# Performance work log

Hardware: AMD Instinct MI355X
Metric: run time of the kernel (lower is better)

## Reference

```python
import jax, jax.numpy as jnp
import numpy as np

B = 65536
N_DIM = 16
K = 64
HIDDEN = 256
IDX_COPIED = np.arange(0, N_DIM, 2)      # mask == 0
IDX_TRANS = np.arange(1, N_DIM, 2)       # mask == 1
T = len(IDX_TRANS)                        # n_dim_transformed = 8
OUT = T * (2 * K + 1)                     # 1032


def setup_inputs() -> dict:
    key = jax.random.key(0)
    ks = jax.random.split(key, 7)
    def lin_init(k, fan_in, shape):
        s = 1.0 / np.sqrt(fan_in)
        return jax.random.uniform(k, shape, minval=-s, maxval=s, dtype=jnp.float32)
    x = jax.random.uniform(ks[0], (B, N_DIM), dtype=jnp.float32)  # inputs in [0,1)
    W1 = lin_init(ks[1], T, (T, HIDDEN)); b1 = lin_init(ks[2], T, (HIDDEN,))
    W2 = lin_init(ks[3], HIDDEN, (HIDDEN, HIDDEN)); b2 = lin_init(ks[4], HIDDEN, (HIDDEN,))
    W3 = lin_init(ks[5], HIDDEN, (HIDDEN, OUT)); b3 = lin_init(ks[6], HIDDEN, (OUT,))
    return {"x": x, "W1": W1, "b1": b1, "W2": W2, "b2": b2, "W3": W3, "b3": b3}


def reference(x, W1, b1, W2, b2, W3, b3):
    xc = x[:, IDX_COPIED]                 # [B, T] copied dims
    xt = x[:, IDX_TRANS]                  # [B, T] transformed dims
    # FCNN as built by torch: Linear, Linear, ReLU, Linear (no ReLU after 1st)
    h = xc @ W1 + b1
    h = jax.nn.relu(h @ W2 + b2)
    params = h @ W3 + b3                  # [B, T*(2K+1)]

    Vun = params[:, : T * (K + 1)].reshape(B, T, K + 1)
    Wun = params[:, T * (K + 1):].reshape(B, T, K)
    Wb = jax.nn.softmax(Wun, axis=-1)     # bin widths [B,T,K]

    expV = jnp.exp(Vun)                   # [B,T,K+1]
    denom = jnp.sum(0.5 * (expV[..., :-1] + expV[..., 1:]) * Wb, axis=-1, keepdims=True)
    V = expV / denom                      # normalized vertex heights [B,T,K+1]

    Wcum = jnp.cumsum(Wb, axis=-1)        # [B,T,K]
    b = jnp.argmax((Wcum > xt[..., None]).astype(jnp.int32), axis=-1, keepdims=True)  # bin index [B,T,1]
    Wcum_pad = jnp.pad(Wcum, ((0, 0), (0, 0), (1, 0)))

    g = lambda a, idx: jnp.take_along_axis(a, idx, axis=-1)
    Wb_b = g(Wb, b)
    alpha = (xt[..., None] - g(Wcum_pad, b)) / Wb_b   # relative position in bin

    Cint = 0.5 * (V[..., :-1] + V[..., 1:]) * Wb      # per-bin CDF mass [B,T,K]
    Cint_cum = jnp.pad(jnp.cumsum(Cint, axis=-1), ((0, 0), (0, 0), (1, 0)))

    Vb = g(V, b); Vb1 = g(V, b + 1)
    C = (0.5 * alpha**2 * (Vb1 - Vb) * Wb_b + alpha * Vb * Wb_b + g(Cint_cum, b))[..., 0]  # [B,T]

    z = jnp.zeros_like(x).at[:, IDX_COPIED].set(xc).at[:, IDX_TRANS].set(C)
    z = jnp.where(z > 1.0, 1.0, z)

    q = Vb + alpha * (Vb1 - Vb)           # linear interp of density
    log_J = jnp.sum(jnp.log(q)[..., 0], axis=-1)      # [B]
    return z, log_J
```

## Files before the change

kernel.cpp:

```cpp
#include <hip/hip_runtime.h>

typedef short s16x8 __attribute__((ext_vector_type(8)));
typedef float fx4 __attribute__((ext_vector_type(4)));

#define NROWS 65536
#define LOG2E 1.4426950408889634f
#define LN2   0.6931471805599453f

#define MFMA(a, b, c) __builtin_amdgcn_mfma_f32_16x16x32_bf16((a), (b), (c), 0, 0, 0)

__device__ __forceinline__ unsigned short f2bf(float f) {
  union { float f; unsigned u; } v; v.f = f;
  unsigned r = v.u + 0x7fffu + ((v.u >> 16) & 1u);
  return (unsigned short)(r >> 16);
}

__device__ __forceinline__ float fexp2(float x) {
  float r; asm("v_exp_f32 %0, %1" : "=v"(r) : "v"(x)); return r;
}
__device__ __forceinline__ float flog2(float x) {
  float r; asm("v_log_f32 %0, %1" : "=v"(r) : "v"(x)); return r;
}
__device__ __forceinline__ float frcp(float x) {
  float r; asm("v_rcp_f32 %0, %1" : "=v"(r) : "v"(x)); return r;
}

__global__ void pack_weights(const float* __restrict__ W1, const float* __restrict__ b1,
                             const float* __restrict__ W2, const float* __restrict__ b2,
                             const float* __restrict__ W3,
                             unsigned short* __restrict__ W12P, float* __restrict__ b12,
                             unsigned short* __restrict__ W3Q, unsigned short* __restrict__ W3X) {
  int blk = blockIdx.x, tid = threadIdx.x;
  if (blk < 1024) {
    int i3 = blk * 256 + tid;
    int e = i3 & 7, lane = (i3 >> 3) & 63, nti = (i3 >> 9) & 7, ks = (i3 >> 12) & 7, t = i3 >> 15;
    int m = lane & 15, kc = lane >> 4;
    int k = ks * 32 + kc * 8 + e;
    int g = m >> 2, rg = m & 3;
    int c = (nti < 4) ? (t * 65 + 16 * g + nti * 4 + rg)
                      : (520 + t * 64 + 16 * g + (nti - 4) * 4 + rg);
    W3Q[i3] = f2bf(W3[k * 1032 + c] * LOG2E);
  } else if (blk < 1040) {
    int ix = (blk - 1024) * 256 + tid;
    int e = ix & 7, n = (ix >> 3) & 15, kc = (ix >> 7) & 3, ks = ix >> 9;
    int k = ks * 32 + kc * 8 + e;
    float v = (n < 8) ? (W3[k * 1032 + n * 65 + 64] * LOG2E) : 0.0f;
    W3X[ix] = f2bf(v);
  } else if (blk < 1048) {
    int k = blk - 1040, c = tid;
    float s = 0.0f;
    for (int m = 0; m < 256; m++) s += W1[k * 256 + m] * W2[m * 256 + c];
    W12P[c * 8 + k] = f2bf(s);
  } else {
    int c = tid;
    float s = b2[c];
    for (int m = 0; m < 256; m++) s += b1[m] * W2[m * 256 + c];
    b12[c] = s;
  }
}

__global__ __launch_bounds__(256, 2) void fused_pwquad(
    const float* __restrict__ x, const float* __restrict__ b3,
    const unsigned short* __restrict__ W12P, const float* __restrict__ b12,
    const unsigned short* __restrict__ W3Q, const unsigned short* __restrict__ W3X,
    float* __restrict__ out)
{
  __shared__ char smem_all[75776];
  const int tid  = threadIdx.x;
  const int w    = tid >> 6;
  const int lane = tid & 63;
  const int kc   = lane >> 4;
  const int l15  = lane & 15;
  const int r0   = blockIdx.x * 128 + w * 32;

  char*  smem  = smem_all + w * 18944;
  char*  H     = smem;
  float* b3V   = (float*)smem;
  float* b3W   = (float*)(smem + 2176);
  char*  XC    = smem + 16384;
  float* xt_s  = (float*)(smem + 16896);
  float* v64_s = (float*)(smem + 17920);

  {
    const float4* xin = (const float4*)(x + (size_t)r0 * 16);
    #pragma unroll
    for (int i = 0; i < 2; i++) {
      int f = i * 64 + lane;
      float4 v = xin[f];
      int row = f >> 2, q = f & 3;
      out[(size_t)(r0 + row) * 16 + 4 * q + 0] = fminf(v.x, 1.0f);
      out[(size_t)(r0 + row) * 16 + 4 * q + 2] = fminf(v.z, 1.0f);
      unsigned pk = (unsigned)f2bf(v.x) | ((unsigned)f2bf(v.z) << 16);
      *(unsigned*)(XC + row * 16 + q * 4) = pk;
      float2 t2; t2.x = v.y; t2.y = v.w;
      *(float2*)(xt_s + row * 8 + 2 * q) = t2;
    }
  }

  {
    s16x8 ah[2] = {};
    if (kc == 0) {
      #pragma unroll
      for (int mi = 0; mi < 2; mi++) ah[mi] = *(const s16x8*)(XC + (mi * 16 + l15) * 16);
    }
    #pragma unroll
    for (int c = 0; c < 4; c++) {
      s16x8 bh[4];
      #pragma unroll
      for (int nt = 0; nt < 4; nt++)
        bh[nt] = *(const s16x8*)(W12P + (size_t)(c * 64 + nt * 16 + l15) * 8);
      fx4 acc[2][4];
      #pragma unroll
      for (int mi = 0; mi < 2; mi++)
        #pragma unroll
        for (int nt = 0; nt < 4; nt++) acc[mi][nt] = (fx4){0.f, 0.f, 0.f, 0.f};
      #pragma unroll
      for (int mi = 0; mi < 2; mi++)
        #pragma unroll
        for (int nt = 0; nt < 4; nt++) acc[mi][nt] = MFMA(ah[mi], bh[nt], acc[mi][nt]);
      #pragma unroll
      for (int nt = 0; nt < 4; nt++) {
        int col = c * 64 + nt * 16 + l15;
        float bias = b12[col];
        #pragma unroll
        for (int mi = 0; mi < 2; mi++) {
          #pragma unroll
          for (int rg = 0; rg < 4; rg++) {
            int row = mi * 16 + kc * 4 + rg;
            float v = fmaxf(acc[mi][nt][rg] + bias, 0.0f);
            int byte = (row << 9) + (col << 1);
            byte ^= ((row & 7) << 4);
            *(unsigned short*)(H + byte) = f2bf(v);
          }
        }
      }
    }
  }

  s16x8 a3[2][8];
  #pragma unroll
  for (int mi = 0; mi < 2; mi++) {
    #pragma unroll
    for (int ks = 0; ks < 8; ks++) {
      int row = mi * 16 + l15;
      int byte = (row << 9) + ks * 64 + (kc << 4);
      byte ^= ((row & 7) << 4);
      a3[mi][ks] = *(const s16x8*)(H + byte);
    }
  }
  {
    fx4 ax0 = (fx4){0.f, 0.f, 0.f, 0.f}, ax1 = ax0;
    #pragma unroll
    for (int ks = 0; ks < 8; ks++) {
      s16x8 bx = *(const s16x8*)(W3X + ((size_t)(ks * 4 + kc) * 16 + l15) * 8);
      ax0 = MFMA(a3[0][ks], bx, ax0);
      ax1 = MFMA(a3[1][ks], bx, ax1);
    }
    if (l15 < 8) {
      float bias = b3[l15 * 65 + 64] * LOG2E;
      #pragma unroll
      for (int rg = 0; rg < 4; rg++) {
        v64_s[(kc * 4 + rg) * 8 + l15]      = ax0[rg] + bias;
        v64_s[(16 + kc * 4 + rg) * 8 + l15] = ax1[rg] + bias;
      }
    }
  }

  #pragma unroll
  for (int t = 0; t < 8; t++) {
    b3V[t * 68 + lane] = b3[t * 65 + lane] * LOG2E;
    b3W[t * 64 + lane] = b3[520 + t * 64 + lane] * LOG2E;
  }

  const char* wp = (const char*)W3Q + (size_t)lane * 16;

  s16x8 F0[8], F1[8];
  #pragma unroll
  for (int nti = 0; nti < 8; nti++) F0[nti] = *(const s16x8*)(wp + nti * 1024);

  float ljacc[2] = {0.0f, 0.0f};
  const fx4 Z = (fx4){0.f, 0.f, 0.f, 0.f};

  #pragma unroll 1
  for (int t = 0; t < 8; t++) {
    const char* wk = wp + (size_t)t * 65536;

    fx4 accT[8][2];

    {
      #pragma unroll
      for (int nti = 0; nti < 8; nti++) F1[nti] = *(const s16x8*)(wk + 8192 + nti * 1024);
      __builtin_amdgcn_s_setprio(1);
      #pragma unroll
      for (int nti = 0; nti < 8; nti++) {
        accT[nti][0] = MFMA(F0[nti], a3[0][0], Z);
        accT[nti][1] = MFMA(F0[nti], a3[1][0], Z);
      }
      __builtin_amdgcn_s_setprio(0);
      #pragma unroll
      for (int nti = 0; nti < 8; nti++) F0[nti] = *(const s16x8*)(wk + 16384 + nti * 1024);
      __builtin_amdgcn_s_setprio(1);
      #pragma unroll
      for (int nti = 0; nti < 8; nti++) {
        accT[nti][0] = MFMA(F1[nti], a3[0][1], accT[nti][0]);
        accT[nti][1] = MFMA(F1[nti], a3[1][1], accT[nti][1]);
      }
      __builtin_amdgcn_s_setprio(0);
    }
    #pragma unroll
    for (int kp = 1; kp < 4; kp++) {
      const char* e0 = wk + kp * 16384;
      #pragma unroll
      for (int nti = 0; nti < 8; nti++) F1[nti] = *(const s16x8*)(e0 + 8192 + nti * 1024);
      __builtin_amdgcn_s_setprio(1);
      #pragma unroll
      for (int nti = 0; nti < 8; nti++) {
        accT[nti][0] = MFMA(F0[nti], a3[0][2 * kp], accT[nti][0]);
        accT[nti][1] = MFMA(F0[nti], a3[1][2 * kp], accT[nti][1]);
      }
      __builtin_amdgcn_s_setprio(0);
      if (kp < 3 || t < 7) {
        #pragma unroll
        for (int nti = 0; nti < 8; nti++) F0[nti] = *(const s16x8*)(e0 + 16384 + nti * 1024);
      }
      __builtin_amdgcn_s_setprio(1);
      #pragma unroll
      for (int nti = 0; nti < 8; nti++) {
        accT[nti][0] = MFMA(F1[nti], a3[0][2 * kp + 1], accT[nti][0]);
        accT[nti][1] = MFMA(F1[nti], a3[1][2 * kp + 1], accT[nti][1]);
      }
      __builtin_amdgcn_s_setprio(0);
    }

    fx4 vb[4], wb[4];
    {
      const float* bV = b3V + t * 68 + 16 * kc;
      const float* bW = b3W + t * 64 + 16 * kc;
      #pragma unroll
      for (int i = 0; i < 4; i++) { vb[i] = *(const fx4*)(bV + 4 * i); wb[i] = *(const fx4*)(bW + 4 * i); }
    }
    float xtv_p[2], vlast_p[2];
    xtv_p[0]   = xt_s[l15 * 8 + t];        xtv_p[1]   = xt_s[(16 + l15) * 8 + t];
    vlast_p[0] = v64_s[l15 * 8 + t];       vlast_p[1] = v64_s[(16 + l15) * 8 + t];

    #pragma unroll
    for (int mi = 0; mi < 2; mi++) {
      int row = mi * 16 + l15;
      float xtv   = xtv_p[mi];
      float vlast = vlast_p[mi];

      float wj[16];
      #pragma unroll
      for (int i = 0; i < 4; i++)
        #pragma unroll
        for (int j = 0; j < 4; j++)
          wj[4 * i + j] = fexp2(accT[4 + i][mi][j] + wb[i][j]);

      float esum = 0.0f;
      #pragma unroll
      for (int j = 0; j < 16; j++) esum += wj[j];

      float g0 = __shfl(esum, l15, 64);
      float g1 = __shfl(esum, l15 + 16, 64);
      float g2 = __shfl(esum, l15 + 32, 64);
      float g3 = __shfl(esum, l15 + 48, 64);
      float S = (g0 + g1) + (g2 + g3);
      float ebase = 0.0f;
      if (kc > 0) ebase += g0;
      if (kc > 1) ebase += g1;
      if (kc > 2) ebase += g2;
      float xs = xtv * S;

      float v0my = accT[0][mi][0] + vb[0][0];
      float vnext = __shfl(v0my, l15 + (((kc + 1) & 3) << 4), 64);
      if (kc == 3) vnext = vlast;

      float run = ebase;
      float evc = fexp2(v0my);
      float dl = 0.0f, cpart = 0.0f;
      float wpadc = 0.0f, wbbc = 1.0f, evb = evc, evb1 = evc;
      float ev15 = evc, ev16 = evc;
      int jcap = 16;
      #pragma unroll
      for (int j = 0; j < 16; j++) {
        float vr = (j < 15) ? (accT[(j + 1) >> 2][mi][(j + 1) & 3] + vb[(j + 1) >> 2][(j + 1) & 3])
                            : vnext;
        float evn = fexp2(vr);
        float wbj = wj[j];
        float nw = run + wbj;
        bool hit = (run <= xs) && (nw > xs);
        if (hit) { wpadc = run; wbbc = wbj; evb = evc; evb1 = evn; cpart = dl; jcap = j; }
        dl += (evc + evn) * wbj;
        if (j == 15) { ev15 = evc; ev16 = evn; }
        run = nw; evc = evn;
      }
      int bloc = (jcap < 16) ? (kc * 16 + jcap) : 64;
      int bmin = min(bloc, __shfl_xor(bloc, 16, 64));
      bmin = min(bmin, __shfl_xor(bmin, 32, 64));

      float d0 = __shfl(dl, l15, 64);
      float d1 = __shfl(dl, l15 + 16, 64);
      float d2 = __shfl(dl, l15 + 32, 64);
      float d3 = __shfl(dl, l15 + 48, 64);
      float dltot = (d0 + d1) + (d2 + d3);
      float cbase2 = 0.0f;
      if (kc > 0) cbase2 += d0;
      if (kc > 1) cbase2 += d1;
      if (kc > 2) cbase2 += d2;

      if (bmin == 64) {
        wbbc = wj[15];
        wpadc = run - wbbc;
        evb = ev15; evb1 = ev16;
        cpart = dl - (ev15 + ev16) * wj[15];
        bmin = 63;
      }

      if (kc == (bmin >> 4)) {
        float alpha = (xs - wpadc) * frcp(wbbc);
        float Cnum = (alpha * (evb + 0.5f * alpha * (evb1 - evb))) * wbbc
                   + 0.5f * (cbase2 + cpart);
        out[(size_t)(r0 + row) * 16 + 2 * t + 1] = fminf(2.0f * Cnum * frcp(dltot), 1.0f);
        float qn = evb + alpha * (evb1 - evb);
        ljacc[mi] += flog2(qn) - (flog2(dltot) - 1.0f - flog2(S));
      }
    }
  }

  #pragma unroll
  for (int mi = 0; mi < 2; mi++) {
    float v = ljacc[mi];
    v += __shfl_xor(v, 16, 64);
    v += __shfl_xor(v, 32, 64);
    if (kc == 0) out[(size_t)NROWS * 16 + r0 + mi * 16 + l15] = v * LN2;
  }
}

extern "C" void kernel_launch(void* const* d_in, const int* in_sizes, int n_in,
                              void* d_out, int out_size, void* d_ws, size_t ws_size,
                              hipStream_t stream) {
  const float* x  = (const float*)d_in[0];
  const float* W1 = (const float*)d_in[1];
  const float* b1 = (const float*)d_in[2];
  const float* W2 = (const float*)d_in[3];
  const float* b2 = (const float*)d_in[4];
  const float* W3 = (const float*)d_in[5];
  const float* b3 = (const float*)d_in[6];

  unsigned short* W12P = (unsigned short*)d_ws;
  float*          b12  = (float*)((char*)d_ws + 4096);
  unsigned short* W3Q  = (unsigned short*)((char*)d_ws + 5120);
  unsigned short* W3X  = (unsigned short*)((char*)d_ws + 529408);

  pack_weights<<<dim3(1049), dim3(256), 0, stream>>>(W1, b1, W2, b2, W3, W12P, b12, W3Q, W3X);
  fused_pwquad<<<dim3(NROWS / 128), dim3(256), 0, stream>>>(
      x, b3, W12P, b12, W3Q, W3X, (float*)d_out);
}
```

Baseline: 56.95 us.

## Stage W3 weight fragments through double-buffered LDS shared across the block's waves

Before, each of the four waves streamed its own copy of the packed W3 bf16 fragments from global memory into registers for the final-layer MFMA loop. Now the block loads each 8 KB k-slice once, cooperatively at 32 bytes per thread, into one of two LDS buffers. Each slice is prefetched two steps ahead into registers, and the waves read their MFMA fragments from LDS. This removes the 4x redundant global/L2 weight traffic per block. In exchange it adds a block-wide barrier after every k-step (64 per block) and extra LDS traffic, and it reuses LDS space left by the finished hidden-activation stage as the two buffers.

```diff
diff --git a/kernel.cpp b/kernel.cpp
--- a/kernel.cpp
+++ b/kernel.cpp
@@ -23,6 +23,10 @@
 }
 __device__ __forceinline__ float frcp(float x) {
   float r; asm("v_rcp_f32 %0, %1" : "=v"(r) : "v"(x)); return r;
+}
+
+__device__ __forceinline__ void bar_lds() {
+  asm volatile("s_waitcnt lgkmcnt(0)\n\ts_barrier" ::: "memory");
 }
 
 __global__ void pack_weights(const float* __restrict__ W1, const float* __restrict__ b1,
@@ -65,7 +69,7 @@
     const unsigned short* __restrict__ W3Q, const unsigned short* __restrict__ W3X,
     float* __restrict__ out)
 {
-  __shared__ char smem_all[75776];
+  __shared__ __attribute__((aligned(128))) char smem_all[75776];
   const int tid  = threadIdx.x;
   const int w    = tid >> 6;
   const int lane = tid & 63;
@@ -80,6 +84,8 @@
   char*  XC    = smem + 16384;
   float* xt_s  = (float*)(smem + 16896);
   float* v64_s = (float*)(smem + 17920);
+  char*  S0    = smem_all + 8192;
+  char*  S1    = smem_all + 18944 + 8192;
 
   {
     const float4* xin = (const float4*)(x + (size_t)r0 * 16);
@@ -172,64 +178,72 @@
     b3W[t * 64 + lane] = b3[520 + t * 64 + lane] * LOG2E;
   }
 
-  const char* wp = (const char*)W3Q + (size_t)lane * 16;
-
-  s16x8 F0[8], F1[8];
-  #pragma unroll
-  for (int nti = 0; nti < 8; nti++) F0[nti] = *(const s16x8*)(wp + nti * 1024);
+  bar_lds();
+
+  const char* W3Qb = (const char*)W3Q;
+  const int gofs = tid * 32;
+  {
+    s16x8 a0 = *(const s16x8*)(W3Qb + gofs);
+    s16x8 a1 = *(const s16x8*)(W3Qb + gofs + 16);
+    *(s16x8*)(S0 + gofs) = a0;
+    *(s16x8*)(S0 + gofs + 16) = a1;
+  }
+  s16x8 PA0, PA1, PB0, PB1;
+  PB0 = *(const s16x8*)(W3Qb + 8192 + gofs);
+  PB1 = *(const s16x8*)(W3Qb + 8192 + gofs + 16);
+  bar_lds();
 
   float ljacc[2] = {0.0f, 0.0f};
   const fx4 Z = (fx4){0.f, 0.f, 0.f, 0.f};
 
   #pragma unroll 1
   for (int t = 0; t < 8; t++) {
-    const char* wk = wp + (size_t)t * 65536;
+    const char* wkt = W3Qb + (size_t)t * 65536 + gofs;
 
     fx4 accT[8][2];
 
-    {
-      #pragma unroll
-      for (int nti = 0; nti < 8; nti++) F1[nti] = *(const s16x8*)(wk + 8192 + nti * 1024);
+    #pragma unroll
+    for (int ks = 0; ks < 8; ks++) {
+      if (t < 7 || ks < 6) {
+        if ((ks & 1) == 0) {
+          PA0 = *(const s16x8*)(wkt + (ks + 2) * 8192);
+          PA1 = *(const s16x8*)(wkt + (ks + 2) * 8192 + 16);
+        } else {
+          PB0 = *(const s16x8*)(wkt + (ks + 2) * 8192);
+          PB1 = *(const s16x8*)(wkt + (ks + 2) * 8192 + 16);
+        }
+      }
+      const char* Ssrc = (ks & 1) ? S1 : S0;
+      s16x8 F[8];
+      #pragma unroll
+      for (int nti = 0; nti < 8; nti++)
+        F[nti] = *(const s16x8*)(Ssrc + nti * 1024 + lane * 16);
       __builtin_amdgcn_s_setprio(1);
-      #pragma unroll
-      for (int nti = 0; nti < 8; nti++) {
-        accT[nti][0] = MFMA(F0[nti], a3[0][0], Z);
-        accT[nti][1] = MFMA(F0[nti], a3[1][0], Z);
+      if (ks == 0) {
+        #pragma unroll
+        for (int nti = 0; nti < 8; nti++) {
+          accT[nti][0] = MFMA(F[nti], a3[0][0], Z);
+          accT[nti][1] = MFMA(F[nti], a3[1][0], Z);
+        }
+      } else {
+        #pragma unroll
+        for (int nti = 0; nti < 8; nti++) {
+          accT[nti][0] = MFMA(F[nti], a3[0][ks], accT[nti][0]);
+          accT[nti][1] = MFMA(F[nti], a3[1][ks], accT[nti][1]);
+        }
       }
       __builtin_amdgcn_s_setprio(0);
-      #pragma unroll
-      for (int nti = 0; nti < 8; nti++) F0[nti] = *(const s16x8*)(wk + 16384 + nti * 1024);
-      __builtin_amdgcn_s_setprio(1);
-      #pragma unroll
-      for (int nti = 0; nti < 8; nti++) {
-        accT[nti][0] = MFMA(F1[nti], a3[0][1], accT[nti][0]);
-        accT[nti][1] = MFMA(F1[nti], a3[1][1], accT[nti][1]);
-      }
-      __builtin_amdgcn_s_setprio(0);
-    }
-    #pragma unroll
-    for (int kp = 1; kp < 4; kp++) {
-      const char* e0 = wk + kp * 16384;
-      #pragma unroll
-      for (int nti = 0; nti < 8; nti++) F1[nti] = *(const s16x8*)(e0 + 8192 + nti * 1024);
-      __builtin_amdgcn_s_setprio(1);
-      #pragma unroll
-      for (int nti = 0; nti < 8; nti++) {
-        accT[nti][0] = MFMA(F0[nti], a3[0][2 * kp], accT[nti][0]);
-        accT[nti][1] = MFMA(F0[nti], a3[1][2 * kp], accT[nti][1]);
-      }
-      __builtin_amdgcn_s_setprio(0);
-      if (kp < 3 || t < 7) {
-        #pragma unroll
-        for (int nti = 0; nti < 8; nti++) F0[nti] = *(const s16x8*)(e0 + 16384 + nti * 1024);
-      }
-      __builtin_amdgcn_s_setprio(1);
-      #pragma unroll
-      for (int nti = 0; nti < 8; nti++) {
-        accT[nti][0] = MFMA(F1[nti], a3[0][2 * kp + 1], accT[nti][0]);
-        accT[nti][1] = MFMA(F1[nti], a3[1][2 * kp + 1], accT[nti][1]);
-      }
-      __builtin_amdgcn_s_setprio(0);
+      if (t < 7 || ks < 7) {
+        char* Sdst = (ks & 1) ? S0 : S1;
+        if ((ks & 1) == 0) {
+          *(s16x8*)(Sdst + gofs) = PB0;
+          *(s16x8*)(Sdst + gofs + 16) = PB1;
+        } else {
+          *(s16x8*)(Sdst + gofs) = PA0;
+          *(s16x8*)(Sdst + gofs + 16) = PA1;
+        }
+      }
+      bar_lds();
     }
 
     fx4 vb[4], wb[4];
```

New measurement: 59.21 us. +4.0%, slower.
